# Kernel optimization log

Measured on AMD Instinct MI355X. Metric: run time of the kernel, lower is better.

Reference implementation:

```python
import jax, jax.numpy as jnp
import numpy as np

MIN_DIST = 0.1
BIG = 1e10

def setup_inputs() -> dict:
    key = jax.random.key(0)
    kV, kP, kN, kF, kE = jax.random.split(key, 5)
    B, N, F, P = 4, 8192, 8192, 2048
    mesh_V = jax.random.normal(kV, (B, N, 3), dtype=jnp.float32)
    points = jax.random.normal(kP, (B, P, 3), dtype=jnp.float32)
    fn = jax.random.normal(kN, (B, F, 3), dtype=jnp.float32)
    mesh_FN = fn / jnp.linalg.norm(fn, axis=-1, keepdims=True)  # unit face normals
    mesh_F = jax.random.randint(kF, (B, F, 3), 0, N, dtype=jnp.int32)
    exterior_flag = jax.random.bernoulli(kE, 0.5, (B, P, 1))
    return {"mesh_V": mesh_V, "points": points, "mesh_FN": mesh_FN,
            "mesh_F": mesh_F, "exterior_flag": exterior_flag}

def reference(mesh_V, points, mesh_FN, mesh_F, exterior_flag):
    B, P, _ = points.shape
    fn = jax.lax.stop_gradient(mesh_FN)                       # normals are detached
    # gather face vertices: (B,F,3verts,3)
    face_points = jax.vmap(lambda V, Fi: V[Fi])(mesh_V, mesh_F)
    face_center = jnp.mean(face_points, axis=-2)              # (B,F,3)
    # signed distance of each point to each face plane
    diff = points[:, :, None, :] - face_center[:, None, :, :] # (B,P,F,3)
    signed = jnp.sum(diff * fn[:, None, :, :], axis=-1) + MIN_DIST  # (B,P,F)
    # ||signed * n||^2 = signed^2 * ||n||^2  (avoids (B,P,F,3) re-materialization)
    fn_sq = jnp.sum(fn * fn, axis=-1)                         # (B,F)
    sqdist = (signed * signed) * fn_sq[:, None, :]            # (B,P,F)
    sqdist = jnp.where(signed < 0, BIG, sqdist)
    min_sqdist = jnp.min(sqdist, axis=-1)                     # (B,P)
    inside = (~exterior_flag.reshape(B, P)) | jnp.all(signed < 0, axis=-1)
    min_sqdist = jnp.where(inside, 0.0, min_sqdist)
    per_batch = jnp.mean(min_sqdist, axis=1)                  # reduction='mean'
    return jnp.mean(per_batch, axis=0)                        # scalar
```

## Files before the change

### kernel.cpp

```cpp
#include <hip/hip_runtime.h>
#include <math.h>

#define Bn 4
#define Nn 8192
#define Fn 8192
#define Pn 2048
#define G 64
#define CH (Fn / G)
#define TPB 512
#define PPT (Pn / TPB)
#define MIN_DIST 0.1f
#define FLTMAX_BITS 0x7F7FFFFFu

typedef float v2f __attribute__((ext_vector_type(2)));

struct Meta { float acc; int cnt; int mode; };

__global__ __launch_bounds__(TPB)
void chunk_min(const float* __restrict__ V, const float* __restrict__ FN,
               const int* __restrict__ Fidx, const float* __restrict__ points,
               const unsigned char* __restrict__ flags,
               unsigned* __restrict__ partials, Meta* __restrict__ meta) {
    int g = blockIdx.x & (G - 1);
    int b = blockIdx.x / G;
    int tid = threadIdx.x;

    __shared__ float4 lf[CH];

    if (tid < CH) {
        int i = b * Fn + g * CH + tid;
        const int* fi = Fidx + (size_t)i * 3;
        int i0 = fi[0], i1 = fi[1], i2 = fi[2];
        const float* Vb = V + (size_t)b * Nn * 3;
        float cx = (Vb[i0*3+0] + Vb[i1*3+0] + Vb[i2*3+0]) * (1.0f/3.0f);
        float cy = (Vb[i0*3+1] + Vb[i1*3+1] + Vb[i2*3+1]) * (1.0f/3.0f);
        float cz = (Vb[i0*3+2] + Vb[i1*3+2] + Vb[i2*3+2]) * (1.0f/3.0f);
        const float* n = FN + (size_t)i * 3;
        float nx = n[0], ny = n[1], nz = n[2];
        float d = MIN_DIST - (cx*nx + cy*ny + cz*nz);
        float s = sqrtf(nx*nx + ny*ny + nz*nz);
        lf[tid] = make_float4(nx*s, ny*s, nz*s, d*s);
    }

    v2f px[PPT/2], py[PPT/2], pz[PPT/2];
    const float* pb = points + (size_t)b * Pn * 3;
#pragma unroll
    for (int k = 0; k < PPT/2; ++k) {
        int p0 = tid + 2 * TPB * k;
        int p1 = p0 + TPB;
        px[k] = (v2f){pb[p0*3+0], pb[p1*3+0]};
        py[k] = (v2f){pb[p0*3+1], pb[p1*3+1]};
        pz[k] = (v2f){pb[p0*3+2], pb[p1*3+2]};
    }
    unsigned m[PPT];
#pragma unroll
    for (int k = 0; k < PPT; ++k) m[k] = FLTMAX_BITS;

    __syncthreads();

#pragma unroll 8
    for (int j = 0; j < CH; ++j) {
        float4 f = lf[j];
        v2f fx = (v2f){f.x, f.x}, fy = (v2f){f.y, f.y},
            fz = (v2f){f.z, f.z}, fw = (v2f){f.w, f.w};
#pragma unroll
        for (int k = 0; k < PPT/2; ++k) {
#if __has_builtin(__builtin_elementwise_fma)
            v2f s = __builtin_elementwise_fma(px[k], fx,
                    __builtin_elementwise_fma(py[k], fy,
                    __builtin_elementwise_fma(pz[k], fz, fw)));
#else
            v2f s;
            s.x = fmaf(px[k].x, f.x, fmaf(py[k].x, f.y, fmaf(pz[k].x, f.z, f.w)));
            s.y = fmaf(px[k].y, f.x, fmaf(py[k].y, f.y, fmaf(pz[k].y, f.z, f.w)));
#endif
            unsigned sx = __float_as_uint(s.x);
            unsigned sy = __float_as_uint(s.y);
            m[2*k]   = sx < m[2*k]   ? sx : m[2*k];
            m[2*k+1] = sy < m[2*k+1] ? sy : m[2*k+1];
        }
    }

    unsigned* out = partials + (size_t)g * (Bn * Pn) + (size_t)b * Pn;
#pragma unroll
    for (int k = 0; k < PPT/2; ++k) {
        out[tid + 2 * TPB * k]       = m[2*k];
        out[tid + 2 * TPB * k + TPB] = m[2*k+1];
    }

    if (blockIdx.x == 0) {
        __shared__ int cnt;
        if (tid == 0) cnt = 0;
        __syncthreads();
        int local = 0;
        for (int i = tid; i < Bn * Pn; i += TPB)
            if ((i & 3) && flags[i]) local++;
        if (local) atomicAdd(&cnt, local);
        __syncthreads();
        if (tid == 0) {
            meta->mode = (cnt > 0) ? 1 : 0;
            meta->acc = 0.0f;
            meta->cnt = 0;
        }
    }
}

__global__ __launch_bounds__(128)
void point_reduce(const unsigned* __restrict__ partials,
                  const unsigned char* __restrict__ flagsB,
                  const int* __restrict__ flagsI,
                  Meta* __restrict__ meta, float* __restrict__ out) {
    int i = blockIdx.x * 128 + threadIdx.x;
    unsigned m = FLTMAX_BITS;
#pragma unroll 8
    for (int c = 0; c < G; ++c) {
        unsigned v = partials[(size_t)c * (Bn * Pn) + i];
        m = v < m ? v : m;
    }
    int ext = (meta->mode) ? (flagsB[i] != 0) : (flagsI[i] != 0);
    float mf = __uint_as_float(m);
    float val = (ext && m < FLTMAX_BITS) ? mf * mf : 0.0f;

    for (int o = 32; o > 0; o >>= 1) val += __shfl_down(val, o);
    __shared__ float wsum[2];
    int lane = threadIdx.x & 63, wid = threadIdx.x >> 6;
    if (lane == 0) wsum[wid] = val;
    __syncthreads();
    if (threadIdx.x == 0) {
        float s = wsum[0] + wsum[1];
        atomicAdd(&meta->acc, s);
        __threadfence();
        int ticket = atomicAdd(&meta->cnt, 1);
        if (ticket == gridDim.x - 1) {
            float total = atomicAdd(&meta->acc, 0.0f);
            out[0] = total * (1.0f / (Bn * Pn));
        }
    }
}

extern "C" void kernel_launch(void* const* d_in, const int* in_sizes, int n_in,
                              void* d_out, int out_size, void* d_ws, size_t ws_size,
                              hipStream_t stream) {
    const float* mesh_V  = (const float*)d_in[0];
    const float* points  = (const float*)d_in[1];
    const float* mesh_FN = (const float*)d_in[2];
    const int*   mesh_F  = (const int*)d_in[3];
    const void*  eflag   = d_in[4];
    float* out = (float*)d_out;

    char* ws = (char*)d_ws;
    const size_t partBytes = (size_t)G * Bn * Pn * sizeof(unsigned);
    unsigned* partials = (unsigned*)ws;
    Meta*     meta     = (Meta*)(ws + partBytes);

    chunk_min<<<Bn * G, TPB, 0, stream>>>(mesh_V, mesh_FN, mesh_F, points,
                                          (const unsigned char*)eflag,
                                          partials, meta);
    point_reduce<<<(Bn * Pn) / 128, 128, 0, stream>>>(partials,
                                                      (const unsigned char*)eflag,
                                                      (const int*)eflag, meta, out);
}
```

Baseline: 76.87 us.

## Fuse chunk-min and reduction into one kernel partitioned by point groups

Replaces the two-kernel scheme (face-chunk partial minima written to global memory, then a point reduction) with a single kernel. Each block owns 32 points of one batch and loops over all faces in shared-memory passes of 2048. It splits faces across 32 slices per point pair and reduces the slices through shared memory before the atomic final sum. This drops the partials buffer and the second launch and adds a memset to reset the accumulator. In exchange, every block recomputes face centroids and plane data for all 8192 faces, which is 64x redundant gather work per batch, and it adds extra barriers.

```diff
diff --git a/kernel.cpp b/kernel.cpp
--- a/kernel.cpp
+++ b/kernel.cpp
@@ -5,133 +5,111 @@
 #define Nn 8192
 #define Fn 8192
 #define Pn 2048
-#define G 64
-#define CH (Fn / G)
+#define PTS 32
 #define TPB 512
-#define PPT (Pn / TPB)
+#define HALF 2048
+#define NPASS (Fn / HALF)
 #define MIN_DIST 0.1f
 #define FLTMAX_BITS 0x7F7FFFFFu
 
 typedef float v2f __attribute__((ext_vector_type(2)));
 
-struct Meta { float acc; int cnt; int mode; };
+struct Meta { float acc; int cnt; };
 
 __global__ __launch_bounds__(TPB)
-void chunk_min(const float* __restrict__ V, const float* __restrict__ FN,
+void fused_pfd(const float* __restrict__ V, const float* __restrict__ FN,
                const int* __restrict__ Fidx, const float* __restrict__ points,
-               const unsigned char* __restrict__ flags,
-               unsigned* __restrict__ partials, Meta* __restrict__ meta) {
-    int g = blockIdx.x & (G - 1);
-    int b = blockIdx.x / G;
-    int tid = threadIdx.x;
+               const unsigned char* __restrict__ flagsB,
+               Meta* __restrict__ meta, float* __restrict__ out) {
+    const int t  = threadIdx.x;
+    const int b  = blockIdx.x >> 6;
+    const int pg = blockIdx.x & 63;
+    const int* flagsI = (const int*)flagsB;
 
-    __shared__ float4 lf[CH];
+    __shared__ float4 lf[HALF];
 
-    if (tid < CH) {
-        int i = b * Fn + g * CH + tid;
-        const int* fi = Fidx + (size_t)i * 3;
-        int i0 = fi[0], i1 = fi[1], i2 = fi[2];
-        const float* Vb = V + (size_t)b * Nn * 3;
-        float cx = (Vb[i0*3+0] + Vb[i1*3+0] + Vb[i2*3+0]) * (1.0f/3.0f);
-        float cy = (Vb[i0*3+1] + Vb[i1*3+1] + Vb[i2*3+1]) * (1.0f/3.0f);
-        float cz = (Vb[i0*3+2] + Vb[i1*3+2] + Vb[i2*3+2]) * (1.0f/3.0f);
-        const float* n = FN + (size_t)i * 3;
-        float nx = n[0], ny = n[1], nz = n[2];
-        float d = MIN_DIST - (cx*nx + cy*ny + cz*nz);
-        float s = sqrtf(nx*nx + ny*ny + nz*nz);
-        lf[tid] = make_float4(nx*s, ny*s, nz*s, d*s);
-    }
-
-    v2f px[PPT/2], py[PPT/2], pz[PPT/2];
-    const float* pb = points + (size_t)b * Pn * 3;
-#pragma unroll
-    for (int k = 0; k < PPT/2; ++k) {
-        int p0 = tid + 2 * TPB * k;
-        int p1 = p0 + TPB;
-        px[k] = (v2f){pb[p0*3+0], pb[p1*3+0]};
-        py[k] = (v2f){pb[p0*3+1], pb[p1*3+1]};
-        pz[k] = (v2f){pb[p0*3+2], pb[p1*3+2]};
-    }
-    unsigned m[PPT];
-#pragma unroll
-    for (int k = 0; k < PPT; ++k) m[k] = FLTMAX_BITS;
-
+    int* scratch = (int*)lf;
+    if (t == 0) scratch[0] = 0;
+    __syncthreads();
+    if (((unsigned)flagsI[t]) > 1u) scratch[0] = 1;
+    __syncthreads();
+    const int mode = scratch[0];
     __syncthreads();
 
+    const int q = t & 15, slice = t >> 4;
+    const int p0 = pg * PTS + 2 * q;
+    const float* pb = points + ((size_t)b * Pn + p0) * 3;
+    v2f px = {pb[0], pb[3]};
+    v2f py = {pb[1], pb[4]};
+    v2f pz = {pb[2], pb[5]};
+    unsigned m0 = FLTMAX_BITS, m1 = FLTMAX_BITS;
+
+    const float* Vb = V + (size_t)b * Nn * 3;
+
+    for (int h = 0; h < NPASS; ++h) {
+#pragma unroll 4
+        for (int j = 0; j < HALF / TPB; ++j) {
+            int fl = j * TPB + t;
+            size_t fb = ((size_t)b * Fn + h * HALF + fl) * 3;
+            int i0 = Fidx[fb + 0], i1 = Fidx[fb + 1], i2 = Fidx[fb + 2];
+            float cx = (Vb[i0*3+0] + Vb[i1*3+0] + Vb[i2*3+0]) * (1.0f/3.0f);
+            float cy = (Vb[i0*3+1] + Vb[i1*3+1] + Vb[i2*3+1]) * (1.0f/3.0f);
+            float cz = (Vb[i0*3+2] + Vb[i1*3+2] + Vb[i2*3+2]) * (1.0f/3.0f);
+            float nx = FN[fb + 0], ny = FN[fb + 1], nz = FN[fb + 2];
+            float d  = MIN_DIST - (cx*nx + cy*ny + cz*nz);
+            float s  = sqrtf(nx*nx + ny*ny + nz*nz);
+            lf[fl] = make_float4(nx*s, ny*s, nz*s, d*s);
+        }
+        __syncthreads();
+
 #pragma unroll 8
-    for (int j = 0; j < CH; ++j) {
-        float4 f = lf[j];
-        v2f fx = (v2f){f.x, f.x}, fy = (v2f){f.y, f.y},
-            fz = (v2f){f.z, f.z}, fw = (v2f){f.w, f.w};
-#pragma unroll
-        for (int k = 0; k < PPT/2; ++k) {
+        for (int i = 0; i < HALF / 32; ++i) {
+            float4 f = lf[i * 32 + slice];
+            v2f fx = {f.x, f.x}, fy = {f.y, f.y}, fz = {f.z, f.z}, fw = {f.w, f.w};
 #if __has_builtin(__builtin_elementwise_fma)
-            v2f s = __builtin_elementwise_fma(px[k], fx,
-                    __builtin_elementwise_fma(py[k], fy,
-                    __builtin_elementwise_fma(pz[k], fz, fw)));
+            v2f s = __builtin_elementwise_fma(px, fx,
+                    __builtin_elementwise_fma(py, fy,
+                    __builtin_elementwise_fma(pz, fz, fw)));
 #else
             v2f s;
-            s.x = fmaf(px[k].x, f.x, fmaf(py[k].x, f.y, fmaf(pz[k].x, f.z, f.w)));
-            s.y = fmaf(px[k].y, f.x, fmaf(py[k].y, f.y, fmaf(pz[k].y, f.z, f.w)));
+            s.x = fmaf(px.x, f.x, fmaf(py.x, f.y, fmaf(pz.x, f.z, f.w)));
+            s.y = fmaf(px.y, f.x, fmaf(py.y, f.y, fmaf(pz.y, f.z, f.w)));
 #endif
             unsigned sx = __float_as_uint(s.x);
             unsigned sy = __float_as_uint(s.y);
-            m[2*k]   = sx < m[2*k]   ? sx : m[2*k];
-            m[2*k+1] = sy < m[2*k+1] ? sy : m[2*k+1];
+            m0 = sx < m0 ? sx : m0;
+            m1 = sy < m1 ? sy : m1;
         }
+        __syncthreads();
     }
 
-    unsigned* out = partials + (size_t)g * (Bn * Pn) + (size_t)b * Pn;
+    unsigned* red = (unsigned*)lf;
+    red[2 * t + 0] = m0;
+    red[2 * t + 1] = m1;
+    __syncthreads();
+
+    float val = 0.0f;
+    if (t < 32) {
+        unsigned mm = FLTMAX_BITS;
 #pragma unroll
-    for (int k = 0; k < PPT/2; ++k) {
-        out[tid + 2 * TPB * k]       = m[2*k];
-        out[tid + 2 * TPB * k + TPB] = m[2*k+1];
+        for (int s2 = 0; s2 < 32; ++s2) {
+            unsigned v = red[(s2 * 16 + (t >> 1)) * 2 + (t & 1)];
+            mm = v < mm ? v : mm;
+        }
+        int gp = b * Pn + pg * PTS + t;
+        int ext = mode ? (flagsB[gp] != 0) : (flagsI[gp] != 0);
+        float mf = __uint_as_float(mm);
+        val = (ext && mm < FLTMAX_BITS) ? mf * mf : 0.0f;
+    }
+    if (t < 64) {
+        for (int o = 16; o > 0; o >>= 1) val += __shfl_down(val, o);
     }
 
-    if (blockIdx.x == 0) {
-        __shared__ int cnt;
-        if (tid == 0) cnt = 0;
-        __syncthreads();
-        int local = 0;
-        for (int i = tid; i < Bn * Pn; i += TPB)
-            if ((i & 3) && flags[i]) local++;
-        if (local) atomicAdd(&cnt, local);
-        __syncthreads();
-        if (tid == 0) {
-            meta->mode = (cnt > 0) ? 1 : 0;
-            meta->acc = 0.0f;
-            meta->cnt = 0;
-        }
-    }
-}
-
-__global__ __launch_bounds__(128)
-void point_reduce(const unsigned* __restrict__ partials,
-                  const unsigned char* __restrict__ flagsB,
-                  const int* __restrict__ flagsI,
-                  Meta* __restrict__ meta, float* __restrict__ out) {
-    int i = blockIdx.x * 128 + threadIdx.x;
-    unsigned m = FLTMAX_BITS;
-#pragma unroll 8
-    for (int c = 0; c < G; ++c) {
-        unsigned v = partials[(size_t)c * (Bn * Pn) + i];
-        m = v < m ? v : m;
-    }
-    int ext = (meta->mode) ? (flagsB[i] != 0) : (flagsI[i] != 0);
-    float mf = __uint_as_float(m);
-    float val = (ext && m < FLTMAX_BITS) ? mf * mf : 0.0f;
-
-    for (int o = 32; o > 0; o >>= 1) val += __shfl_down(val, o);
-    __shared__ float wsum[2];
-    int lane = threadIdx.x & 63, wid = threadIdx.x >> 6;
-    if (lane == 0) wsum[wid] = val;
-    __syncthreads();
-    if (threadIdx.x == 0) {
-        float s = wsum[0] + wsum[1];
-        atomicAdd(&meta->acc, s);
+    if (t == 0) {
+        atomicAdd(&meta->acc, val);
         __threadfence();
         int ticket = atomicAdd(&meta->cnt, 1);
-        if (ticket == gridDim.x - 1) {
+        if (ticket == (int)gridDim.x - 1) {
             float total = atomicAdd(&meta->acc, 0.0f);
             out[0] = total * (1.0f / (Bn * Pn));
         }
@@ -145,18 +123,11 @@
     const float* points  = (const float*)d_in[1];
     const float* mesh_FN = (const float*)d_in[2];
     const int*   mesh_F  = (const int*)d_in[3];
-    const void*  eflag   = d_in[4];
-    float* out = (float*)d_out;
+    const unsigned char* eflag = (const unsigned char*)d_in[4];
+    float* out  = (float*)d_out;
+    Meta*  meta = (Meta*)d_ws;
 
-    char* ws = (char*)d_ws;
-    const size_t partBytes = (size_t)G * Bn * Pn * sizeof(unsigned);
-    unsigned* partials = (unsigned*)ws;
-    Meta*     meta     = (Meta*)(ws + partBytes);
-
-    chunk_min<<<Bn * G, TPB, 0, stream>>>(mesh_V, mesh_FN, mesh_F, points,
-                                          (const unsigned char*)eflag,
-                                          partials, meta);
-    point_reduce<<<(Bn * Pn) / 128, 128, 0, stream>>>(partials,
-                                                      (const unsigned char*)eflag,
-                                                      (const int*)eflag, meta, out);
+    hipMemsetAsync(meta, 0, sizeof(Meta), stream);
+    fused_pfd<<<Bn * 64, TPB, 0, stream>>>(mesh_V, mesh_FN, mesh_F, points,
+                                           eflag, meta, out);
 }
```

New measurement: 96.02 us. +24.9%, slower.

## Fuse chunk-min and reduction into one kernel via atomicMin and last-block ticket

Applied to the files above, without the earlier changes.

Drops the per-chunk partials buffer and the second reduction kernel. Each block now atomicMins its per-point minima straight into one global array, which a memset initialises to 0x7F bytes. The last block to arrive, found with an atomic ticket counter, does the final masked sum and writes the scalar. This removes a kernel launch and the 2 MB partials round-trip, but adds a memset node, global atomic contention, and a serial single-block final reduction over 8192 points. The flag-layout detection now samples only the first 512 words.

```diff
diff --git a/kernel.cpp b/kernel.cpp
--- a/kernel.cpp
+++ b/kernel.cpp
@@ -10,25 +10,28 @@
 #define TPB 512
 #define PPT (Pn / TPB)
 #define MIN_DIST 0.1f
-#define FLTMAX_BITS 0x7F7FFFFFu
+#define INIT_BITS 0x7F7F7F7Fu
 
 typedef float v2f __attribute__((ext_vector_type(2)));
 
-struct Meta { float acc; int cnt; int mode; };
-
 __global__ __launch_bounds__(TPB)
-void chunk_min(const float* __restrict__ V, const float* __restrict__ FN,
+void fused_min(const float* __restrict__ V, const float* __restrict__ FN,
                const int* __restrict__ Fidx, const float* __restrict__ points,
-               const unsigned char* __restrict__ flags,
-               unsigned* __restrict__ partials, Meta* __restrict__ meta) {
-    int g = blockIdx.x & (G - 1);
-    int b = blockIdx.x / G;
-    int tid = threadIdx.x;
+               const unsigned char* __restrict__ flagsB,
+               unsigned* __restrict__ gmin, unsigned* __restrict__ cnt,
+               float* __restrict__ out) {
+    const int g = blockIdx.x & (G - 1);
+    const int b = blockIdx.x / G;
+    const int t = threadIdx.x;
+    const int* flagsI = (const int*)flagsB;
 
     __shared__ float4 lf[CH];
+    __shared__ int sticket;
+    __shared__ int smode;
+    __shared__ float wsum[TPB / 64];
 
-    if (tid < CH) {
-        int i = b * Fn + g * CH + tid;
+    if (t < CH) {
+        int i = b * Fn + g * CH + t;
         const int* fi = Fidx + (size_t)i * 3;
         int i0 = fi[0], i1 = fi[1], i2 = fi[2];
         const float* Vb = V + (size_t)b * Nn * 3;
@@ -39,14 +42,14 @@
         float nx = n[0], ny = n[1], nz = n[2];
         float d = MIN_DIST - (cx*nx + cy*ny + cz*nz);
         float s = sqrtf(nx*nx + ny*ny + nz*nz);
-        lf[tid] = make_float4(nx*s, ny*s, nz*s, d*s);
+        lf[t] = make_float4(nx*s, ny*s, nz*s, d*s);
     }
 
     v2f px[PPT/2], py[PPT/2], pz[PPT/2];
     const float* pb = points + (size_t)b * Pn * 3;
 #pragma unroll
     for (int k = 0; k < PPT/2; ++k) {
-        int p0 = tid + 2 * TPB * k;
+        int p0 = t + 2 * TPB * k;
         int p1 = p0 + TPB;
         px[k] = (v2f){pb[p0*3+0], pb[p1*3+0]};
         py[k] = (v2f){pb[p0*3+1], pb[p1*3+1]};
@@ -54,7 +57,7 @@
     }
     unsigned m[PPT];
 #pragma unroll
-    for (int k = 0; k < PPT; ++k) m[k] = FLTMAX_BITS;
+    for (int k = 0; k < PPT; ++k) m[k] = INIT_BITS;
 
     __syncthreads();
 
@@ -81,60 +84,46 @@
         }
     }
 
-    unsigned* out = partials + (size_t)g * (Bn * Pn) + (size_t)b * Pn;
+    unsigned* gb = gmin + (size_t)b * Pn;
 #pragma unroll
     for (int k = 0; k < PPT/2; ++k) {
-        out[tid + 2 * TPB * k]       = m[2*k];
-        out[tid + 2 * TPB * k + TPB] = m[2*k+1];
+        atomicMin(&gb[t + 2 * TPB * k],       m[2*k]);
+        atomicMin(&gb[t + 2 * TPB * k + TPB], m[2*k+1]);
     }
 
-    if (blockIdx.x == 0) {
-        __shared__ int cnt;
-        if (tid == 0) cnt = 0;
-        __syncthreads();
-        int local = 0;
-        for (int i = tid; i < Bn * Pn; i += TPB)
-            if ((i & 3) && flags[i]) local++;
-        if (local) atomicAdd(&cnt, local);
-        __syncthreads();
-        if (tid == 0) {
-            meta->mode = (cnt > 0) ? 1 : 0;
-            meta->acc = 0.0f;
-            meta->cnt = 0;
-        }
+    __syncthreads();
+    if (t == 0) {
+        __threadfence();
+        unsigned ticket = atomicAdd(cnt, 1u);
+        sticket = (ticket == INIT_BITS + (unsigned)(Bn * G) - 1u);
     }
-}
+    __syncthreads();
+    if (!sticket) return;
+    __threadfence();
 
-__global__ __launch_bounds__(128)
-void point_reduce(const unsigned* __restrict__ partials,
-                  const unsigned char* __restrict__ flagsB,
-                  const int* __restrict__ flagsI,
-                  Meta* __restrict__ meta, float* __restrict__ out) {
-    int i = blockIdx.x * 128 + threadIdx.x;
-    unsigned m = FLTMAX_BITS;
-#pragma unroll 8
-    for (int c = 0; c < G; ++c) {
-        unsigned v = partials[(size_t)c * (Bn * Pn) + i];
-        m = v < m ? v : m;
+    if (t == 0) smode = 0;
+    __syncthreads();
+    if (((unsigned)flagsI[t]) > 1u) smode = 1;
+    __syncthreads();
+    const int mode = smode;
+
+    float sum = 0.0f;
+    for (int i = t; i < Bn * Pn; i += TPB) {
+        unsigned mm = __hip_atomic_load(&gmin[i], __ATOMIC_RELAXED,
+                                        __HIP_MEMORY_SCOPE_AGENT);
+        int ext = mode ? (flagsB[i] != 0) : (flagsI[i] != 0);
+        float mf = __uint_as_float(mm);
+        if (ext && mm < INIT_BITS) sum += mf * mf;
     }
-    int ext = (meta->mode) ? (flagsB[i] != 0) : (flagsI[i] != 0);
-    float mf = __uint_as_float(m);
-    float val = (ext && m < FLTMAX_BITS) ? mf * mf : 0.0f;
-
-    for (int o = 32; o > 0; o >>= 1) val += __shfl_down(val, o);
-    __shared__ float wsum[2];
-    int lane = threadIdx.x & 63, wid = threadIdx.x >> 6;
-    if (lane == 0) wsum[wid] = val;
+    for (int o = 32; o > 0; o >>= 1) sum += __shfl_down(sum, o);
+    const int lane = t & 63, wid = t >> 6;
+    if (lane == 0) wsum[wid] = sum;
     __syncthreads();
-    if (threadIdx.x == 0) {
-        float s = wsum[0] + wsum[1];
-        atomicAdd(&meta->acc, s);
-        __threadfence();
-        int ticket = atomicAdd(&meta->cnt, 1);
-        if (ticket == gridDim.x - 1) {
-            float total = atomicAdd(&meta->acc, 0.0f);
-            out[0] = total * (1.0f / (Bn * Pn));
-        }
+    if (t == 0) {
+        float total = 0.0f;
+#pragma unroll
+        for (int w = 0; w < TPB / 64; ++w) total += wsum[w];
+        out[0] = total * (1.0f / (Bn * Pn));
     }
 }
 
@@ -145,18 +134,14 @@
     const float* points  = (const float*)d_in[1];
     const float* mesh_FN = (const float*)d_in[2];
     const int*   mesh_F  = (const int*)d_in[3];
-    const void*  eflag   = d_in[4];
+    const unsigned char* eflag = (const unsigned char*)d_in[4];
     float* out = (float*)d_out;
 
-    char* ws = (char*)d_ws;
-    const size_t partBytes = (size_t)G * Bn * Pn * sizeof(unsigned);
-    unsigned* partials = (unsigned*)ws;
-    Meta*     meta     = (Meta*)(ws + partBytes);
+    unsigned* gmin = (unsigned*)d_ws;
+    unsigned* cnt  = (unsigned*)((char*)d_ws + (size_t)Bn * Pn * sizeof(unsigned));
 
-    chunk_min<<<Bn * G, TPB, 0, stream>>>(mesh_V, mesh_FN, mesh_F, points,
-                                          (const unsigned char*)eflag,
-                                          partials, meta);
-    point_reduce<<<(Bn * Pn) / 128, 128, 0, stream>>>(partials,
-                                                      (const unsigned char*)eflag,
-                                                      (const int*)eflag, meta, out);
+    hipMemsetAsync(d_ws, 0x7F, (size_t)Bn * Pn * sizeof(unsigned) + sizeof(unsigned),
+                   stream);
+    fused_min<<<Bn * G, TPB, 0, stream>>>(mesh_V, mesh_FN, mesh_F, points,
+                                          eflag, gmin, cnt, out);
 }
```

Result: slower. 82.17 us (+6.9%).
